# Kernel optimization log

Measured on AMD Instinct MI355X. Metric: run time of the kernel, lower is better.

The kernel has to match this reference:

```python
import jax, jax.numpy as jnp
import numpy as np

N_NODES = 100000
N_EDGES = 1600000
IN_C = 128
OUT_C = 128


def setup_inputs() -> dict:
    key = jax.random.key(0)
    k1, k2, k3, k4 = jax.random.split(key, 4)
    x = jax.random.normal(k1, (N_NODES, IN_C), dtype=jnp.float32)
    W = jax.random.normal(k2, (IN_C, OUT_C), dtype=jnp.float32) * (1.0 / np.sqrt(IN_C))
    b = jax.random.normal(k3, (OUT_C,), dtype=jnp.float32) * 0.02
    edge_index = jax.random.randint(k4, (2, N_EDGES), 0, N_NODES, dtype=jnp.int32)
    return {"x": x, "W": W, "b": b, "edge_index": edge_index}


def reference(x, W, b, edge_index):
    N = x.shape[0]
    # Symmetrize edges: concat(edge_index, flip(edge_index)) as in adj()
    row = jnp.concatenate([edge_index[0], edge_index[1]])  # [2E]
    col = jnp.concatenate([edge_index[1], edge_index[0]])  # [2E]
    w = jnp.ones(row.shape, dtype=x.dtype)
    # gcn_norm with self loops (fill value 1): deg includes self-loop weight
    deg = jax.ops.segment_sum(w, row, num_segments=N) + 1.0
    dinv = jnp.where(deg > 0, jax.lax.rsqrt(deg), 0.0)  # [N]
    # Dense linear projection (bias=False)
    xw = x @ W  # [N, out]
    # SpMM: y[row] += dinv[row]*dinv[col] * xw[col]  (scatter-add == coalesced adj matmul)
    norm = dinv[row] * dinv[col]  # [2E]
    msgs = norm[:, None] * xw[col]  # [2E, out] -- dominant memory traffic
    y = jax.ops.segment_sum(msgs, row, num_segments=N)
    # Self-loop contribution: weight dinv[i]^2
    y = y + (dinv * dinv)[:, None] * xw
    return y + b
```

## Files before the change

### kernel.cpp

```cpp
#include <hip/hip_runtime.h>
#include <math.h>

constexpr int N = 100000;
constexpr int E = 1600000;
constexpr int C = 128;
constexpr int NPB   = 256;
constexpr int NBUCK = (N + NPB - 1) / NPB;
constexpr int CAP   = 9472;
constexpr int ADJ_STRIDE = CAP + NPB * 7;
constexpr int NT = (N + 63) / 64;
constexpr int GPAD = 16;

typedef __attribute__((ext_vector_type(8))) short bf16x8;
typedef __attribute__((ext_vector_type(4))) float f32x4;

__device__ inline unsigned f2bf(float f) {
    unsigned u = __float_as_uint(f);
    return (u + 0x7fffu + ((u >> 16) & 1u)) >> 16;
}
__device__ inline unsigned pack2(float lo, float hi) {
    return f2bf(lo) | (f2bf(hi) << 16);
}
__device__ inline float bf_lo(unsigned m) { return __uint_as_float(m << 16); }
__device__ inline float bf_hi(unsigned m) { return __uint_as_float(m & 0xffff0000u); }

__global__ __launch_bounds__(256) void k_bin(const int* __restrict__ ei,
                                             int* __restrict__ gcount,
                                             unsigned* __restrict__ staging,
                                             const float* __restrict__ W,
                                             unsigned short* __restrict__ wfrag,
                                             unsigned* __restrict__ z16) {
    const int t = threadIdx.x;
    if (blockIdx.x < 64) {
        const int i = blockIdx.x * 256 + t;
        const int k = i >> 7, c = i & 127;
        const int ct = c >> 4, lr = c & 15;
        const int kc = k >> 5, lg = (k >> 3) & 3, e = k & 7;
        const int idx = ((ct * 4 + kc) * 64 + lg * 16 + lr) * 8 + e;
        const float f = W[i];
        const unsigned hb = f2bf(f);
        wfrag[idx]         = (unsigned short)hb;
        wfrag[16384 + idx] = (unsigned short)f2bf(f - __uint_as_float(hb << 16));
        if (blockIdx.x == 0 && t < 64) z16[(size_t)N * 64 + t] = 0u;
    }
    __shared__ int cnt[NBUCK];
    const long tile = (long)blockIdx.x * 4096;
    for (int i = t; i < NBUCK; i += 256) cnt[i] = 0;
    __syncthreads();
#pragma unroll
    for (int j = 0; j < 16; ++j) {
        const long e = tile + j * 256 + t;
        if (e < E) {
            const int u = ei[e];
            const int v = ei[E + e];
            atomicAdd(&cnt[u >> 8], 1);
            atomicAdd(&cnt[v >> 8], 1);
        }
    }
    __syncthreads();
    for (int i = t; i < NBUCK; i += 256) {
        const int c = cnt[i];
        cnt[i] = atomicAdd(&gcount[i * GPAD], c);
    }
    __syncthreads();
#pragma unroll
    for (int j = 0; j < 16; ++j) {
        const long e = tile + j * 256 + t;
        if (e < E) {
            const int u = ei[e];
            const int v = ei[E + e];
            const int bu = u >> 8, bv = v >> 8;
            const int pu = atomicAdd(&cnt[bu], 1);
            const int pv = atomicAdd(&cnt[bv], 1);
            staging[(size_t)bu * CAP + pu] = ((unsigned)(u & 255) << 17) | (unsigned)v;
            staging[(size_t)bv * CAP + pv] = ((unsigned)(v & 255) << 17) | (unsigned)u;
        }
    }
}

__global__ __launch_bounds__(512) void k_csr(const unsigned* __restrict__ staging,
                                             const int* __restrict__ gcount,
                                             int* __restrict__ deg,
                                             float* __restrict__ dinv,
                                             int* __restrict__ rowptr,
                                             int* __restrict__ adj) {
    __shared__ int hist[NPB];
    __shared__ int wpart[4];
    const int g = blockIdx.x;
    const int t = threadIdx.x;
    const int lane = t & 63, wid = t >> 6;
    const int cnt = gcount[g * GPAD];
    int* slice = adj + (size_t)g * ADJ_STRIDE;
    for (int i = t; i < NPB; i += 512) hist[i] = 0;
    __syncthreads();
    const unsigned* base = staging + (size_t)g * CAP;
    for (int i = t; i < cnt; i += 512) atomicAdd(&hist[base[i] >> 17], 1);
    __syncthreads();
    const int d  = (t < NPB) ? hist[t] : 0;
    const int pd = (d + 7) & ~7;
    int v = pd;
#pragma unroll
    for (int off = 1; off < 64; off <<= 1) {
        int n = __shfl_up(v, off);
        if (lane >= off) v += n;
    }
    if (lane == 63 && wid < 4) wpart[wid] = v;
    __syncthreads();
    if (t == 0) {
        int r = 0;
#pragma unroll
        for (int w = 0; w < 4; ++w) { int x = wpart[w]; wpart[w] = r; r += x; }
    }
    __syncthreads();
    const int pstart = v - pd + ((wid < 4) ? wpart[wid] : 0);
    if (t < NPB) {
        const int node = g * NPB + t;
        if (node < N) {
            deg[node]    = d;
            dinv[node]   = rsqrtf((float)d + 1.0f);
            rowptr[node] = g * ADJ_STRIDE + pstart;
        }
        for (int i = d; i < pd; ++i) slice[pstart + i] = N;
    }
    __syncthreads();
    if (t < NPB) hist[t] = pstart;
    __syncthreads();
    for (int i = t; i < cnt; i += 512) {
        const unsigned e = base[i];
        const int pos = atomicAdd(&hist[e >> 17], 1);
        slice[pos] = (int)(e & 0x1ffffu);
    }
}

__global__ __launch_bounds__(256) void k_gemm(const float* __restrict__ x,
                                              const unsigned short* __restrict__ wfrag,
                                              const float* __restrict__ dinv,
                                              unsigned* __restrict__ z16) {
    __shared__ unsigned short wlds[32768];
    const int t = threadIdx.x;
    {
        const uint4* src = (const uint4*)wfrag;
        uint4* dst = (uint4*)wlds;
#pragma unroll
        for (int j = 0; j < 16; ++j) dst[t + 256 * j] = src[t + 256 * j];
    }
    __syncthreads();

    const int wid = t >> 6, l = t & 63;
    const int lr = l & 15, lg = l >> 4;
    const unsigned short* wl_hi = wlds + l * 8;
    const unsigned short* wl_lo = wlds + 16384 + l * 8;

    for (int tile = blockIdx.x; tile < NT; tile += gridDim.x) {
        const long node = (long)tile * 64 + wid * 16 + lr;
        const bool nv = node < N;
        const float* xr = x + node * C + lg * 8;

        f32x4 acc[8];
#pragma unroll
        for (int i = 0; i < 8; ++i) acc[i] = (f32x4){0.f, 0.f, 0.f, 0.f};

#pragma unroll
        for (int kc = 0; kc < 4; ++kc) {
            float4 f0 = {0.f, 0.f, 0.f, 0.f}, f1 = {0.f, 0.f, 0.f, 0.f};
            if (nv) {
                f0 = *(const float4*)(xr + kc * 32);
                f1 = *(const float4*)(xr + kc * 32 + 4);
            }
            bf16x8 bh, bl;
#pragma unroll
            for (int e = 0; e < 8; ++e) {
                const float fe = (e < 4) ? (&f0.x)[e] : (&f1.x)[e - 4];
                const unsigned hb = f2bf(fe);
                bh[e] = (short)hb;
                bl[e] = (short)f2bf(fe - __uint_as_float(hb << 16));
            }
#pragma unroll
            for (int ct = 0; ct < 8; ++ct) {
                const int fo = (ct * 4 + kc) * 512;
                const bf16x8 ahi = *(const bf16x8*)(wl_hi + fo);
                const bf16x8 alo = *(const bf16x8*)(wl_lo + fo);
                acc[ct] = __builtin_amdgcn_mfma_f32_16x16x32_bf16(ahi, bh, acc[ct], 0, 0, 0);
                acc[ct] = __builtin_amdgcn_mfma_f32_16x16x32_bf16(ahi, bl, acc[ct], 0, 0, 0);
                acc[ct] = __builtin_amdgcn_mfma_f32_16x16x32_bf16(alo, bh, acc[ct], 0, 0, 0);
            }
        }

        if (nv) {
            const float dv = dinv[node];
#pragma unroll
            for (int ct = 0; ct < 8; ++ct) {
                uint2 pk = {pack2(dv * acc[ct][0], dv * acc[ct][1]),
                            pack2(dv * acc[ct][2], dv * acc[ct][3])};
                *(uint2*)(z16 + node * 64 + ct * 8 + lg * 2) = pk;
            }
        }
    }
}

__global__ __launch_bounds__(256) void k_gather(const int* __restrict__ rowptr,
                                                const int* __restrict__ deg,
                                                const float* __restrict__ dinv,
                                                const int* __restrict__ adj,
                                                const unsigned* __restrict__ z16,
                                                const float* __restrict__ b,
                                                float* __restrict__ out,
                                                int u0, int u1) {
    const int u = u0 + blockIdx.x * 4 + (threadIdx.x >> 6);
    if (u >= u1) return;
    const int lane = threadIdx.x & 63;
    const int d  = __builtin_amdgcn_readfirstlane(deg[u]);
    const int pd = (d + 7) & ~7;
    const int st = __builtin_amdgcn_readfirstlane(rowptr[u]);
    const float du = dinv[u];

    const unsigned ms = z16[((size_t)(unsigned)u << 6) + lane];
    float ax = bf_lo(ms), ay = bf_hi(ms);

    unsigned q0, q1, q2, q3, q4, q5, q6, q7;
    unsigned r0, r1, r2, r3, r4, r5, r6, r7;

#define ZR(j) z16[((size_t)(unsigned)__builtin_amdgcn_readlane(v, (j)) << 6) + lane]
#define LD8(A, p) A##0 = ZR((p) + 0); A##1 = ZR((p) + 1); A##2 = ZR((p) + 2); \
                  A##3 = ZR((p) + 3); A##4 = ZR((p) + 4); A##5 = ZR((p) + 5); \
                  A##6 = ZR((p) + 6); A##7 = ZR((p) + 7);
#define AC8(A) ax += bf_lo(A##0); ay += bf_hi(A##0); ax += bf_lo(A##1); ay += bf_hi(A##1); \
               ax += bf_lo(A##2); ay += bf_hi(A##2); ax += bf_lo(A##3); ay += bf_hi(A##3); \
               ax += bf_lo(A##4); ay += bf_hi(A##4); ax += bf_lo(A##5); ay += bf_hi(A##5); \
               ax += bf_lo(A##6); ay += bf_hi(A##6); ax += bf_lo(A##7); ay += bf_hi(A##7);

    for (int j0 = 0; j0 < pd; j0 += 64) {
        const int cntc = min(64, pd - j0);
        const int v = adj[st + j0 + lane];
        int p = 8;
        LD8(q, 0);
        for (; p + 16 <= cntc; p += 16) {
            LD8(r, p); AC8(q);
            LD8(q, p + 8); AC8(r);
        }
        if (p < cntc) { LD8(r, p); AC8(q); AC8(r); }
        else          { AC8(q); }
    }
#undef ZR
#undef LD8
#undef AC8

    const float2 bb = *(const float2*)(b + 2 * lane);
    float2 o = {fmaf(du, ax, bb.x), fmaf(du, ay, bb.y)};
    *(float2*)(out + (size_t)u * C + 2 * lane) = o;
}

extern "C" void kernel_launch(void* const* d_in, const int* in_sizes, int n_in,
                              void* d_out, int out_size, void* d_ws, size_t ws_size,
                              hipStream_t stream) {
    const float* x  = (const float*)d_in[0];
    const float* W  = (const float*)d_in[1];
    const float* b  = (const float*)d_in[2];
    const int*   ei = (const int*)d_in[3];
    float* out = (float*)d_out;

    char* p = (char*)d_ws;
    unsigned* z16 = (unsigned*)p;
    unsigned* staging = z16;
    p += (size_t)(N + 1) * 64 * sizeof(unsigned);
    int* adj = (int*)p;             p += ((size_t)NBUCK * ADJ_STRIDE + 64) * sizeof(int);
    int* deg = (int*)p;             p += (size_t)N * sizeof(int);
    float* dinv = (float*)p;        p += (size_t)N * sizeof(float);
    int* rowptr = (int*)p;          p += (size_t)(N + 4) * sizeof(int);
    int* gcount = (int*)p;          p += (size_t)NBUCK * GPAD * sizeof(int);
    unsigned short* wfrag = (unsigned short*)p;

    hipMemsetAsync(gcount, 0, (size_t)NBUCK * GPAD * sizeof(int), stream);
    k_bin<<<(E + 4095) / 4096, 256, 0, stream>>>(ei, gcount, staging, W, wfrag, z16);
    k_csr<<<NBUCK, 512, 0, stream>>>(staging, gcount, deg, dinv, rowptr, adj);
    k_gemm<<<512, 256, 0, stream>>>(x, wfrag, dinv, z16);
    const int third = (N + 2) / 3;
    for (int s = 0; s < 3; ++s) {
        const int u0 = s * third;
        const int u1 = (u0 + third < N) ? (u0 + third) : N;
        k_gather<<<(u1 - u0 + 3) / 4, 256, 0, stream>>>(rowptr, deg, dinv, adj, z16, b, out, u0, u1);
    }
}
```

Measured before the change: 304.2 us.

## Restructure GEMM: 512-thread blocks, preload x fragments, loop over column pairs

The GEMM kernel now uses 512-thread blocks covering 128 nodes per tile, with half as many blocks, so each block's 64 KB LDS copy of W serves twice as many rows. The x row is converted to hi/lo bf16 fragments for all K chunks up front, and the MFMA loop is reordered to compute two output column tiles at a time with interleaved independent accumulators. Each column pair is stored right after it finishes, which cuts live accumulator registers from 32 to 8 in exchange for holding all 8 input fragments. The launch bound of 512 threads with a minimum of 4 blocks requests tighter register allocation, but LDS use per block may cap occupancy anyway.

Measured after the change: 379.4 us. 1.25x slower.

```diff
diff --git a/kernel.cpp b/kernel.cpp
--- a/kernel.cpp
+++ b/kernel.cpp
@@ -8,7 +8,6 @@
 constexpr int NBUCK = (N + NPB - 1) / NPB;
 constexpr int CAP   = 9472;
 constexpr int ADJ_STRIDE = CAP + NPB * 7;
-constexpr int NT = (N + 63) / 64;
 constexpr int GPAD = 16;
 
 typedef __attribute__((ext_vector_type(8))) short bf16x8;
@@ -132,17 +131,17 @@
     }
 }
 
-__global__ __launch_bounds__(256) void k_gemm(const float* __restrict__ x,
-                                              const unsigned short* __restrict__ wfrag,
-                                              const float* __restrict__ dinv,
-                                              unsigned* __restrict__ z16) {
+__global__ __launch_bounds__(512, 4) void k_gemm(const float* __restrict__ x,
+                                                 const unsigned short* __restrict__ wfrag,
+                                                 const float* __restrict__ dinv,
+                                                 unsigned* __restrict__ z16) {
     __shared__ unsigned short wlds[32768];
     const int t = threadIdx.x;
     {
         const uint4* src = (const uint4*)wfrag;
         uint4* dst = (uint4*)wlds;
 #pragma unroll
-        for (int j = 0; j < 16; ++j) dst[t + 256 * j] = src[t + 256 * j];
+        for (int j = 0; j < 8; ++j) dst[t + 512 * j] = src[t + 512 * j];
     }
     __syncthreads();
 
@@ -150,16 +149,14 @@
     const int lr = l & 15, lg = l >> 4;
     const unsigned short* wl_hi = wlds + l * 8;
     const unsigned short* wl_lo = wlds + 16384 + l * 8;
-
-    for (int tile = blockIdx.x; tile < NT; tile += gridDim.x) {
-        const long node = (long)tile * 64 + wid * 16 + lr;
+    constexpr int NT2 = (N + 127) / 128;
+
+    for (int tile = blockIdx.x; tile < NT2; tile += gridDim.x) {
+        const long node = (long)tile * 128 + wid * 16 + lr;
         const bool nv = node < N;
         const float* xr = x + node * C + lg * 8;
 
-        f32x4 acc[8];
-#pragma unroll
-        for (int i = 0; i < 8; ++i) acc[i] = (f32x4){0.f, 0.f, 0.f, 0.f};
-
+        bf16x8 bh[4], bl[4];
 #pragma unroll
         for (int kc = 0; kc < 4; ++kc) {
             float4 f0 = {0.f, 0.f, 0.f, 0.f}, f1 = {0.f, 0.f, 0.f, 0.f};
@@ -167,32 +164,39 @@
                 f0 = *(const float4*)(xr + kc * 32);
                 f1 = *(const float4*)(xr + kc * 32 + 4);
             }
-            bf16x8 bh, bl;
 #pragma unroll
             for (int e = 0; e < 8; ++e) {
                 const float fe = (e < 4) ? (&f0.x)[e] : (&f1.x)[e - 4];
                 const unsigned hb = f2bf(fe);
-                bh[e] = (short)hb;
-                bl[e] = (short)f2bf(fe - __uint_as_float(hb << 16));
-            }
-#pragma unroll
-            for (int ct = 0; ct < 8; ++ct) {
-                const int fo = (ct * 4 + kc) * 512;
-                const bf16x8 ahi = *(const bf16x8*)(wl_hi + fo);
-                const bf16x8 alo = *(const bf16x8*)(wl_lo + fo);
-                acc[ct] = __builtin_amdgcn_mfma_f32_16x16x32_bf16(ahi, bh, acc[ct], 0, 0, 0);
-                acc[ct] = __builtin_amdgcn_mfma_f32_16x16x32_bf16(ahi, bl, acc[ct], 0, 0, 0);
-                acc[ct] = __builtin_amdgcn_mfma_f32_16x16x32_bf16(alo, bh, acc[ct], 0, 0, 0);
-            }
-        }
-
-        if (nv) {
-            const float dv = dinv[node];
-#pragma unroll
-            for (int ct = 0; ct < 8; ++ct) {
-                uint2 pk = {pack2(dv * acc[ct][0], dv * acc[ct][1]),
-                            pack2(dv * acc[ct][2], dv * acc[ct][3])};
-                *(uint2*)(z16 + node * 64 + ct * 8 + lg * 2) = pk;
+                bh[kc][e] = (short)hb;
+                bl[kc][e] = (short)f2bf(fe - __uint_as_float(hb << 16));
+            }
+        }
+        const float dv = nv ? dinv[node] : 0.f;
+
+#pragma unroll
+        for (int cp = 0; cp < 4; ++cp) {
+            f32x4 a0 = {0.f, 0.f, 0.f, 0.f}, a1 = {0.f, 0.f, 0.f, 0.f};
+#pragma unroll
+            for (int kc = 0; kc < 4; ++kc) {
+                const int fo0 = ((2 * cp)     * 4 + kc) * 512;
+                const int fo1 = ((2 * cp + 1) * 4 + kc) * 512;
+                const bf16x8 h0 = *(const bf16x8*)(wl_hi + fo0);
+                const bf16x8 o0 = *(const bf16x8*)(wl_lo + fo0);
+                const bf16x8 h1 = *(const bf16x8*)(wl_hi + fo1);
+                const bf16x8 o1 = *(const bf16x8*)(wl_lo + fo1);
+                a0 = __builtin_amdgcn_mfma_f32_16x16x32_bf16(h0, bh[kc], a0, 0, 0, 0);
+                a1 = __builtin_amdgcn_mfma_f32_16x16x32_bf16(h1, bh[kc], a1, 0, 0, 0);
+                a0 = __builtin_amdgcn_mfma_f32_16x16x32_bf16(h0, bl[kc], a0, 0, 0, 0);
+                a1 = __builtin_amdgcn_mfma_f32_16x16x32_bf16(h1, bl[kc], a1, 0, 0, 0);
+                a0 = __builtin_amdgcn_mfma_f32_16x16x32_bf16(o0, bh[kc], a0, 0, 0, 0);
+                a1 = __builtin_amdgcn_mfma_f32_16x16x32_bf16(o1, bh[kc], a1, 0, 0, 0);
+            }
+            if (nv) {
+                uint2 p0 = {pack2(dv * a0[0], dv * a0[1]), pack2(dv * a0[2], dv * a0[3])};
+                uint2 p1 = {pack2(dv * a1[0], dv * a1[1]), pack2(dv * a1[2], dv * a1[3])};
+                *(uint2*)(z16 + node * 64 + (2 * cp)     * 8 + lg * 2) = p0;
+                *(uint2*)(z16 + node * 64 + (2 * cp + 1) * 8 + lg * 2) = p1;
             }
         }
     }
@@ -273,7 +277,7 @@
     hipMemsetAsync(gcount, 0, (size_t)NBUCK * GPAD * sizeof(int), stream);
     k_bin<<<(E + 4095) / 4096, 256, 0, stream>>>(ei, gcount, staging, W, wfrag, z16);
     k_csr<<<NBUCK, 512, 0, stream>>>(staging, gcount, deg, dinv, rowptr, adj);
-    k_gemm<<<512, 256, 0, stream>>>(x, wfrag, dinv, z16);
+    k_gemm<<<256, 512, 0, stream>>>(x, wfrag, dinv, z16);
     const int third = (N + 2) / 3;
     for (int s = 0; s < 3; ++s) {
         const int u0 = s * third;
```
